# Kernel optimization log

Hardware: AMD Instinct MI355X
Metric: run time of the kernel (lower is better)

## Reference

```python
import jax, jax.numpy as jnp
import numpy as np

B, L, C, H = 4, 4096, 1024, 16


def setup_inputs() -> dict:
    key = jax.random.key(0)
    k1, k2, k3 = jax.random.split(key, 3)
    x = jax.random.normal(k1, (B, L, C), dtype=jnp.float32)
    # torch nn.Linear params: weight (out, in), bias (out,)
    W_qkv = jax.random.normal(k2, (3 * C, C), dtype=jnp.float32) * 0.02
    b_qkv = jnp.zeros((3 * C,), dtype=jnp.float32)
    W_out = jax.random.normal(k3, (C, C), dtype=jnp.float32) * 0.02
    b_out = jnp.zeros((C,), dtype=jnp.float32)
    return {"x": x, "W_qkv": W_qkv, "b_qkv": b_qkv, "W_out": W_out,
            "b_out": b_out, "num_heads": H}


def reference(x, W_qkv, b_qkv, W_out, b_out, num_heads):
    # Faithful to the source, INCLUDING its head-axis bug:
    # q,k,v stay (B, L, H, D); attention is computed over the HEAD axis
    # (H x H per token), and the final transpose(1,2).reshape scrambles
    # sequence/head layout exactly as torch does.
    b, l, c = x.shape
    h = num_heads
    d = c // h
    scale = d ** (-0.5)
    qkv = (x @ W_qkv.T + b_qkv).reshape(b, l, 3, h, d)
    q, k, v = qkv[:, :, 0], qkv[:, :, 1], qkv[:, :, 2]  # (B, L, H, D)
    # (B,L,H,D) @ (B,L,D,H) -> (B,L,H,H)
    attn = jnp.einsum('blhd,blgd->blhg', q, k) * scale
    attn = jax.nn.softmax(attn, axis=-1)
    # dropout is identity in eval mode
    out = jnp.einsum('blhg,blgd->blhd', attn, v)      # (B, L, H, D)
    out = jnp.swapaxes(out, 1, 2).reshape(b, l, c)    # torch transpose(1,2).reshape
    return out @ W_out.T + b_out
```

## Files before the change

kernel.cpp:

```cpp
#include <hip/hip_runtime.h>
#include <hip/hip_bf16.h>


typedef __attribute__((ext_vector_type(8))) short bf16x8;
typedef __attribute__((ext_vector_type(4))) float f32x4;

__device__ __forceinline__ float bf2f(unsigned short u) {
    union { unsigned int i; float f; } x;
    x.i = ((unsigned int)u) << 16;
    return x.f;
}
__device__ __forceinline__ unsigned short f2bf(float f) {
    unsigned int u = __float_as_uint(f);
    u = (u + 0x7FFFu + ((u >> 16) & 1u)) >> 16;
    return (unsigned short)u;
}

#define VMCNT4() asm volatile("s_waitcnt vmcnt(4)" ::: "memory")
#define VMCNT0() asm volatile("s_waitcnt vmcnt(0)" ::: "memory")
#define BAR()    __builtin_amdgcn_s_barrier()
#define SCHED0() __builtin_amdgcn_sched_barrier(0)

__global__ __launch_bounds__(256) void cast_all(const float* __restrict__ x,
                                                const float* __restrict__ wq,
                                                const float* __restrict__ wo,
                                                unsigned short* __restrict__ xb,
                                                unsigned short* __restrict__ wqb,
                                                unsigned short* __restrict__ wob) {
    const size_t base = (size_t)blockIdx.x * 2048 + threadIdx.x;
#pragma unroll
    for (int it = 0; it < 8; ++it) {
        size_t i = base + (size_t)it * 256;
        const float4* s; ushort4* d; size_t off;
        if (i < 4194304)      { s = (const float4*)x;  d = (ushort4*)xb;  off = i; }
        else if (i < 4980736) { s = (const float4*)wq; d = (ushort4*)wqb; off = i - 4194304; }
        else                  { s = (const float4*)wo; d = (ushort4*)wob; off = i - 4980736; }
        float4 v = s[off];
        ushort4 o;
        o.x = f2bf(v.x); o.y = f2bf(v.y); o.z = f2bf(v.z); o.w = f2bf(v.w);
        d[off] = o;
    }
}

template<int OUTF32>
__global__ __launch_bounds__(512, 2) void gemm256(const unsigned short* __restrict__ A,
                                                  const unsigned short* __restrict__ B,
                                                  const float* __restrict__ bias,
                                                  unsigned short* __restrict__ Cb,
                                                  float* __restrict__ Cf,
                                                  int M, int N, int K, int NXT) {
    __shared__ __align__(16) unsigned short lds[2][2][2][8192];

    const int tid  = threadIdx.x;
    const int lane = tid & 63;
    const int wave = tid >> 6;
    const int wr = wave >> 2;
    const int wc = wave & 3;
    const int fr = lane & 15;
    const int fq = lane >> 4;
    const int frx = fr & 7;

    const int nwg  = gridDim.x;
    const int orig = blockIdx.x;
    const int wg   = (orig & 7) * (nwg >> 3) + (orig >> 3);
    const int tileM = (wg / NXT) * 256;
    const int tileN = (wg % NXT) * 256;

    const int r8  = tid >> 3;
    const int jsw = (tid & 7) ^ (r8 & 7);
    const unsigned short* Ap = A;
    const unsigned short* Bp = B;

#define STAGE(nb, OPp, HH, ktt) do {                                                   \
    const unsigned short* gb = (OPp) ? Bp : Ap;                                        \
    const int rb = ((OPp) ? tileN : tileM) + (HH) * 128 + r8;                          \
    const unsigned short* s0 = gb + (size_t)rb * K + (ktt) * 64 + jsw * 8;             \
    unsigned short* d0 = &lds[nb][OPp][HH][tid * 8];                                   \
    __builtin_amdgcn_global_load_lds((const __attribute__((address_space(1))) void*)s0,\
        (__attribute__((address_space(3))) void*)d0, 16, 0, 0);                        \
    __builtin_amdgcn_global_load_lds(                                                  \
        (const __attribute__((address_space(1))) void*)(s0 + (size_t)64 * K),          \
        (__attribute__((address_space(3))) void*)(d0 + 4096), 16, 0, 0);               \
} while (0)

#define READ_A(bb, h) do {                                                             \
    _Pragma("unroll") for (int i2 = 0; i2 < 4; ++i2) {                                 \
        const int ar = (wr * 64 + i2 * 16 + fr) * 64;                                  \
        af[i2][0] = *(const bf16x8*)&lds[bb][0][h][ar + ((fq ^ frx) << 3)];            \
        af[i2][1] = *(const bf16x8*)&lds[bb][0][h][ar + (((4 + fq) ^ frx) << 3)];      \
    }                                                                                  \
} while (0)

#define READ_B(bb, g) do {                                                             \
    _Pragma("unroll") for (int j2 = 0; j2 < 2; ++j2) {                                 \
        const int br = (wc * 32 + j2 * 16 + fr) * 64;                                  \
        bfr[2*(g)+j2][0] = *(const bf16x8*)&lds[bb][1][g][br + ((fq ^ frx) << 3)];     \
        bfr[2*(g)+j2][1] = *(const bf16x8*)&lds[bb][1][g][br + (((4 + fq) ^ frx) << 3)];\
    }                                                                                  \
} while (0)

#define MFMA_Q(h, g) do {                                                              \
    __builtin_amdgcn_s_setprio(1);                                                     \
    _Pragma("unroll") for (int i2 = 0; i2 < 4; ++i2)                                   \
    _Pragma("unroll") for (int j2 = 0; j2 < 2; ++j2) {                                 \
        acc[(h)*4+i2][(g)*2+j2] = __builtin_amdgcn_mfma_f32_16x16x32_bf16(             \
            af[i2][0], bfr[2*(g)+j2][0], acc[(h)*4+i2][(g)*2+j2], 0, 0, 0);            \
        acc[(h)*4+i2][(g)*2+j2] = __builtin_amdgcn_mfma_f32_16x16x32_bf16(             \
            af[i2][1], bfr[2*(g)+j2][1], acc[(h)*4+i2][(g)*2+j2], 0, 0, 0);            \
    }                                                                                  \
    __builtin_amdgcn_s_setprio(0);                                                     \
} while (0)

    f32x4 acc[8][4];
#pragma unroll
    for (int i = 0; i < 8; ++i)
#pragma unroll
        for (int j = 0; j < 4; ++j) acc[i][j] = (f32x4){0.f, 0.f, 0.f, 0.f};

    STAGE(0, 0, 0, 0);
    STAGE(0, 1, 0, 0);
    STAGE(0, 1, 1, 0);
    STAGE(0, 0, 1, 0);

    const int NT = K >> 6;
    int cur = 0;
    for (int kt = 0; kt < NT - 1; ++kt) {
        const int nb = cur ^ 1;
        BAR();
        STAGE(nb, 0, 0, kt + 1);
        STAGE(nb, 1, 0, kt + 1);
        VMCNT4();
        BAR();
        SCHED0();
        bf16x8 af[4][2], bfr[4][2];
        READ_A(cur, 0); READ_B(cur, 0); READ_B(cur, 1);
        MFMA_Q(0, 0);
        STAGE(nb, 1, 1, kt + 1);
        STAGE(nb, 0, 1, kt + 1);
        MFMA_Q(0, 1);
        READ_A(cur, 1);
        MFMA_Q(1, 0);
        MFMA_Q(1, 1);
        cur = nb;
    }
    BAR();
    VMCNT0();
    BAR();
    SCHED0();
    {
        bf16x8 af[4][2], bfr[4][2];
        READ_A(cur, 0); READ_B(cur, 0); READ_B(cur, 1);
        MFMA_Q(0, 0);
        MFMA_Q(0, 1);
        READ_A(cur, 1);
        MFMA_Q(1, 0);
        MFMA_Q(1, 1);
    }

#pragma unroll
    for (int i = 0; i < 8; ++i) {
        const int row = tileM + (i >> 2) * 128 + wr * 64 + (i & 3) * 16 + fq * 4;
#pragma unroll
        for (int j = 0; j < 4; ++j) {
            const int col = tileN + (j >> 1) * 128 + wc * 32 + (j & 1) * 16 + fr;
            const float bv = bias[col];
#pragma unroll
            for (int r = 0; r < 4; ++r) {
                const float v = acc[i][j][r] + bv;
                if (OUTF32) Cf[(size_t)(row + r) * N + col] = v;
                else        Cb[(size_t)(row + r) * N + col] = f2bf(v);
            }
        }
    }
#undef STAGE
#undef READ_A
#undef READ_B
#undef MFMA_Q
}

__global__ __launch_bounds__(256) void attn_kernel(const unsigned short* __restrict__ qkv,
                                                   unsigned short* __restrict__ scr) {
    __shared__ __align__(16) unsigned short sbuf[4][3328];
    __shared__ float Pl[4][256];

    const int wave = threadIdx.x >> 6, lane = threadIdx.x & 63;
    const int token = blockIdx.x * 4 + wave;
    const int b = token >> 12, l = token & 4095;

    const unsigned short* src = qkv + (size_t)token * 3072;
    unsigned short* sw = sbuf[wave];
#pragma unroll
    for (int i = 0; i < 2; ++i) {
        const int c = lane + i * 64;
        const int row = c >> 3, j8 = (c & 7) * 8;
        *(bf16x8*)&sw[row * 72 + j8]        = *(const bf16x8*)&src[c * 8];
        *(bf16x8*)&sw[1152 + row * 72 + j8] = *(const bf16x8*)&src[1024 + c * 8];
        *(bf16x8*)&sw[2304 + c * 8]         = *(const bf16x8*)&src[2048 + c * 8];
    }
    __syncthreads();

    float sv[4];
#pragma unroll
    for (int r = 0; r < 4; ++r) {
        const int p = r * 64 + lane;
        const int h = p >> 4, g = p & 15;
        float acc = 0.f;
#pragma unroll
        for (int d8 = 0; d8 < 8; ++d8) {
            bf16x8 qa = *(const bf16x8*)&sw[h * 72 + d8 * 8];
            bf16x8 kb = *(const bf16x8*)&sw[1152 + g * 72 + d8 * 8];
#pragma unroll
            for (int j = 0; j < 8; ++j)
                acc += bf2f((unsigned short)qa[j]) * bf2f((unsigned short)kb[j]);
        }
        sv[r] = acc * 0.125f;
    }

#pragma unroll
    for (int r = 0; r < 4; ++r) {
        float m = sv[r];
        m = fmaxf(m, __shfl_xor(m, 1));
        m = fmaxf(m, __shfl_xor(m, 2));
        m = fmaxf(m, __shfl_xor(m, 4));
        m = fmaxf(m, __shfl_xor(m, 8));
        float e = __expf(sv[r] - m);
        float s = e;
        s += __shfl_xor(s, 1);
        s += __shfl_xor(s, 2);
        s += __shfl_xor(s, 4);
        s += __shfl_xor(s, 8);
        Pl[wave][r * 64 + lane] = e / s;
    }
    __syncthreads();

    float vreg[16];
#pragma unroll
    for (int g = 0; g < 16; ++g) vreg[g] = bf2f(sw[2304 + g * 64 + lane]);

    const int q_ = l >> 4, j = l & 15;
    const size_t base = ((size_t)b * 4096 + q_) * 1024 + j * 64 + lane;
#pragma unroll
    for (int h = 0; h < 16; ++h) {
        float acc = 0.f;
#pragma unroll
        for (int g = 0; g < 16; ++g) acc += Pl[wave][h * 16 + g] * vreg[g];
        scr[base + (size_t)h * 256 * 1024] = f2bf(acc);
    }
}

extern "C" void kernel_launch(void* const* d_in, const int* in_sizes, int n_in,
                              void* d_out, int out_size, void* d_ws, size_t ws_size,
                              hipStream_t stream) {
    const float* x    = (const float*)d_in[0];
    const float* Wqkv = (const float*)d_in[1];
    const float* bqkv = (const float*)d_in[2];
    const float* Wout = (const float*)d_in[3];
    const float* bout = (const float*)d_in[4];
    float* out = (float*)d_out;

    char* ws = (char*)d_ws;
    unsigned short* xb   = (unsigned short*)(ws);
    unsigned short* wqb  = (unsigned short*)(ws + 33554432);
    unsigned short* wob  = (unsigned short*)(ws + 39845888);
    unsigned short* qkvb = (unsigned short*)(ws + 41943040);
    unsigned short* scr  = (unsigned short*)(ws + 142606336);

    cast_all<<<2560, 256, 0, stream>>>(x, Wqkv, Wout, xb, wqb, wob);

    gemm256<0><<<768, 512, 0, stream>>>(xb, wqb, bqkv, qkvb, nullptr, 16384, 3072, 1024, 12);

    attn_kernel<<<4096, 256, 0, stream>>>(qkvb, scr);

    gemm256<1><<<256, 512, 0, stream>>>(scr, wob, bout, nullptr, out, 16384, 1024, 1024, 4);
}
```

Baseline: 196.0 us.

## Stagger GEMM wave read/MFMA order and use shuffles for softmax probs in attention

In the GEMM main loop, waves in the second row group now process the A half-tiles in reversed order. This staggers LDS reads and MFMA issue across waves to reduce LDS bank and port contention. Separately, the attention kernel drops its shared-memory probability buffer and the block barrier that guarded it. Unnormalized exponentials and reciprocal sums stay in registers and are broadcast with lane shuffles, with normalization applied after the weighted sum. The shuffle approach adds 17 cross-lane ops per output head in exchange for removing the LDS round trip and sync.

After: 234.5 us. 19.6% more time.

```diff
diff --git a/kernel.cpp b/kernel.cpp
--- a/kernel.cpp
+++ b/kernel.cpp
@@ -59,6 +59,7 @@
     const int fr = lane & 15;
     const int fq = lane >> 4;
     const int frx = fr & 7;
+    const int rot = (wave >> 2) & 1;
 
     const int nwg  = gridDim.x;
     const int orig = blockIdx.x;
@@ -133,14 +134,25 @@
         BAR();
         SCHED0();
         bf16x8 af[4][2], bfr[4][2];
-        READ_A(cur, 0); READ_B(cur, 0); READ_B(cur, 1);
-        MFMA_Q(0, 0);
-        STAGE(nb, 1, 1, kt + 1);
-        STAGE(nb, 0, 1, kt + 1);
-        MFMA_Q(0, 1);
-        READ_A(cur, 1);
-        MFMA_Q(1, 0);
-        MFMA_Q(1, 1);
+        if (rot == 0) {
+            READ_A(cur, 0); READ_B(cur, 0); READ_B(cur, 1);
+            MFMA_Q(0, 0);
+            STAGE(nb, 1, 1, kt + 1);
+            STAGE(nb, 0, 1, kt + 1);
+            MFMA_Q(0, 1);
+            READ_A(cur, 1);
+            MFMA_Q(1, 0);
+            MFMA_Q(1, 1);
+        } else {
+            READ_A(cur, 1); READ_B(cur, 0); READ_B(cur, 1);
+            MFMA_Q(1, 0);
+            STAGE(nb, 1, 1, kt + 1);
+            STAGE(nb, 0, 1, kt + 1);
+            MFMA_Q(1, 1);
+            READ_A(cur, 0);
+            MFMA_Q(0, 0);
+            MFMA_Q(0, 1);
+        }
         cur = nb;
     }
     BAR();
@@ -149,12 +161,21 @@
     SCHED0();
     {
         bf16x8 af[4][2], bfr[4][2];
-        READ_A(cur, 0); READ_B(cur, 0); READ_B(cur, 1);
-        MFMA_Q(0, 0);
-        MFMA_Q(0, 1);
-        READ_A(cur, 1);
-        MFMA_Q(1, 0);
-        MFMA_Q(1, 1);
+        if (rot == 0) {
+            READ_A(cur, 0); READ_B(cur, 0); READ_B(cur, 1);
+            MFMA_Q(0, 0);
+            MFMA_Q(0, 1);
+            READ_A(cur, 1);
+            MFMA_Q(1, 0);
+            MFMA_Q(1, 1);
+        } else {
+            READ_A(cur, 1); READ_B(cur, 0); READ_B(cur, 1);
+            MFMA_Q(1, 0);
+            MFMA_Q(1, 1);
+            READ_A(cur, 0);
+            MFMA_Q(0, 0);
+            MFMA_Q(0, 1);
+        }
     }
 
 #pragma unroll
@@ -181,7 +202,6 @@
 __global__ __launch_bounds__(256) void attn_kernel(const unsigned short* __restrict__ qkv,
                                                    unsigned short* __restrict__ scr) {
     __shared__ __align__(16) unsigned short sbuf[4][3328];
-    __shared__ float Pl[4][256];
 
     const int wave = threadIdx.x >> 6, lane = threadIdx.x & 63;
     const int token = blockIdx.x * 4 + wave;
@@ -216,6 +236,7 @@
         sv[r] = acc * 0.125f;
     }
 
+    float ev[4], rs[4];
 #pragma unroll
     for (int r = 0; r < 4; ++r) {
         float m = sv[r];
@@ -229,9 +250,9 @@
         s += __shfl_xor(s, 2);
         s += __shfl_xor(s, 4);
         s += __shfl_xor(s, 8);
-        Pl[wave][r * 64 + lane] = e / s;
-    }
-    __syncthreads();
+        ev[r] = e;
+        rs[r] = 1.0f / s;
+    }
 
     float vreg[16];
 #pragma unroll
@@ -241,10 +262,12 @@
     const size_t base = ((size_t)b * 4096 + q_) * 1024 + j * 64 + lane;
 #pragma unroll
     for (int h = 0; h < 16; ++h) {
+        const int rr = h >> 2, lb = (h & 3) << 4;
         float acc = 0.f;
 #pragma unroll
-        for (int g = 0; g < 16; ++g) acc += Pl[wave][h * 16 + g] * vreg[g];
-        scr[base + (size_t)h * 256 * 1024] = f2bf(acc);
+        for (int g = 0; g < 16; ++g) acc += __shfl(ev[rr], lb + g) * vreg[g];
+        const float o = acc * __shfl(rs[rr], lb);
+        scr[base + (size_t)h * 256 * 1024] = f2bf(o);
     }
 }
 
```
